# Kernel tuning notes

Hardware: AMD Instinct MI355X
Metric: run time of the kernel (lower is better)

Reference implementation:

```python
import jax, jax.numpy as jnp
import numpy as np

B, N, K = 32, 64, 128          # batch, atoms per cell, channel width (128x0e + 128x1o)
R_MAX = 5.0
NUM_BESSEL = 8
P_CUT = 5                       # num_polynomial_cutoff
AVG_NEIGH = 16.0                # avg_num_neighbors
H_MLP = 512                     # hidden_dimensions_size, n_hidden_dimensions = 2
FEAT = 5 * K                    # ((num_interactions-1)*4 + 1) * 128 = 640


def silu(x):
    return x * jax.nn.sigmoid(x)


def _bessel_cutoff(r, mask):
    # Bessel radial basis * polynomial cutoff (MACE), masked on valid edges.
    n = jnp.arange(1, NUM_BESSEL + 1, dtype=r.dtype)
    rb = jnp.sqrt(2.0 / R_MAX) * jnp.sin(n * (jnp.pi / R_MAX) * r[..., None]) / r[..., None]
    u = r / R_MAX
    p = float(P_CUT)
    fc = 1.0 - 0.5 * (p + 1) * (p + 2) * u**P_CUT + p * (p + 2) * u**(P_CUT + 1) - 0.5 * p * (p + 1) * u**(P_CUT + 2)
    fc = fc * (u < 1.0)
    return rb * (fc * mask)[..., None]


def _sph(uvec):
    # Real spherical harmonics l=0,1,2 (component normalization), uvec: unit edge vectors.
    x, y, z = uvec[..., 0], uvec[..., 1], uvec[..., 2]
    s3, s5, s15 = 3.0**0.5, 5.0**0.5, 15.0**0.5
    Y0 = jnp.ones_like(x)[..., None]
    Y1 = jnp.stack([s3 * x, s3 * y, s3 * z], -1)
    Y2 = jnp.stack([s15 * x * y, s15 * y * z, 0.5 * s5 * (3 * z * z - 1.0),
                    s15 * x * z, 0.5 * s15 * (x * x - y * y)], -1)
    return Y0, Y1, Y2


def _radial_mlp(x, w0, b0, w1, b1, w2, b2, w3, b3):
    h = silu(x @ w0 + b0)
    h = silu(h @ w1 + b1)
    h = silu(h @ w2 + b2)
    return h @ w3 + b3


def setup_inputs() -> dict:
    key = jax.random.key(0)
    ks = jax.random.split(key, 32)
    f32 = jnp.float32

    def lin(k, fan_in, shape):
        return (jax.random.normal(k, shape, dtype=f32) / np.sqrt(fan_in)).astype(f32)

    inp = {
        "noisy_relative_positions": jax.random.uniform(ks[0], (B, N, 3), dtype=f32),
        "time": jax.random.uniform(ks[1], (B, 1), dtype=f32),
        "unit_cell": (11.0 * jnp.eye(3, dtype=f32) + 0.3 * jax.random.uniform(ks[2], (B, 3, 3), dtype=f32)),
        "w_embed": lin(ks[3], 1, (K,)),
        # interaction 1 radial MLP: 8 -> 64 -> 64 -> 64 -> 3*K (weights for l=0,1,2 paths)
        "r1_w0": lin(ks[4], NUM_BESSEL, (NUM_BESSEL, 64)), "r1_b0": jnp.zeros((64,), f32),
        "r1_w1": lin(ks[5], 64, (64, 64)), "r1_b1": jnp.zeros((64,), f32),
        "r1_w2": lin(ks[6], 64, (64, 64)), "r1_b2": jnp.zeros((64,), f32),
        "r1_w3": lin(ks[7], 64, (64, 3 * K)), "r1_b3": jnp.zeros((3 * K,), f32),
        "mix1_l0": lin(ks[8], K, (K, K)),
        "mix1_l1": lin(ks[9], K, (K, K)),
        "mix1_l2": lin(ks[10], K, (K, K)),
        # interaction 2 radial MLP: 8 -> 64 -> 64 -> 64 -> 2*K (paths 0e x 0e -> 0e, 1o x 1o -> 0e)
        "r2_w0": lin(ks[11], NUM_BESSEL, (NUM_BESSEL, 64)), "r2_b0": jnp.zeros((64,), f32),
        "r2_w1": lin(ks[12], 64, (64, 64)), "r2_b1": jnp.zeros((64,), f32),
        "r2_w2": lin(ks[13], 64, (64, 64)), "r2_b2": jnp.zeros((64,), f32),
        "r2_w3": lin(ks[14], 64, (64, 2 * K)), "r2_b3": jnp.zeros((2 * K,), f32),
        "mix2": lin(ks[15], K, (K, K)),
        # readout MLP: 641 -> 512 -> 512 -> 3
        "mlp_w0": lin(ks[16], FEAT + 1, (FEAT + 1, H_MLP)), "mlp_b0": jnp.zeros((H_MLP,), f32),
        "mlp_w1": lin(ks[17], H_MLP, (H_MLP, H_MLP)), "mlp_b1": jnp.zeros((H_MLP,), f32),
        "mlp_w2": lin(ks[18], H_MLP, (H_MLP, 3)), "mlp_b2": jnp.zeros((3,), f32),
    }
    return inp


def reference(noisy_relative_positions, time, unit_cell, w_embed,
              r1_w0, r1_b0, r1_w1, r1_b1, r1_w2, r1_b2, r1_w3, r1_b3,
              mix1_l0, mix1_l1, mix1_l2,
              r2_w0, r2_b0, r2_w1, r2_b1, r2_w2, r2_b2, r2_w3, r2_b3, mix2,
              mlp_w0, mlp_b0, mlp_w1, mlp_b1, mlp_w2, mlp_b2):
    frac = noisy_relative_positions                      # [B,N,3] fractional
    d = frac[:, :, None, :] - frac[:, None, :, :]        # [B,N,N,3]
    d = d - jnp.round(d)                                 # minimum-image PBC
    dc = jnp.einsum('bijc,bcd->bijd', d, unit_cell)      # cartesian displacements
    r = jnp.sqrt(jnp.maximum(jnp.sum(dc * dc, -1), 1e-12))
    mask = (r < R_MAX) & (~jnp.eye(N, dtype=bool))[None]
    r_safe = jnp.where(mask, r, 1.0)
    uvec = dc / r_safe[..., None] * mask[..., None]      # unit edge vectors (0 off-edge)

    rad = _bessel_cutoff(r_safe, mask)                   # [B,N,N,8]
    Y0, Y1, Y2 = _sph(uvec)                              # [B,N,N,1|3|5]

    h0 = jnp.broadcast_to(w_embed, (B, N, K))            # element embedding (single species)

    # ---- interaction 1: radial-weighted tensor product h_j (x) Y_l, scatter over j ----
    we = _radial_mlp(rad, r1_w0, r1_b0, r1_w1, r1_b1, r1_w2, r1_b2, r1_w3, r1_b3)
    we = we.reshape(B, N, N, 3, K) * mask[..., None, None]
    hj = h0[:, None, :, :]                               # sender features [B,1,N,K]
    msg0 = jnp.einsum('bijk,bijm->bimk', we[..., 0, :] * hj, Y0)[:, :, 0] / AVG_NEIGH  # [B,N,K]
    msg1 = jnp.einsum('bijk,bijm->bimk', we[..., 1, :] * hj, Y1) / AVG_NEIGH           # [B,N,3,K]
    msg2 = jnp.einsum('bijk,bijm->bimk', we[..., 2, :] * hj, Y2) / AVG_NEIGH           # [B,N,5,K]

    s1 = msg0 @ mix1_l0 + jnp.sum(msg2 * msg2, axis=2) @ mix1_l2   # scalars [B,N,K]
    v1 = jnp.einsum('bimk,kc->bimc', msg1, mix1_l1)                # vectors [B,N,3,K]
    h1 = silu(s1)

    # ---- interaction 2: scalar output from 0e x 0e and 1o x 1o -> 0e paths ----
    we2 = _radial_mlp(rad, r2_w0, r2_b0, r2_w1, r2_b1, r2_w2, r2_b2, r2_w3, r2_b3)
    we2 = we2.reshape(B, N, N, 2, K) * mask[..., None, None]
    msg_a = jnp.sum(we2[..., 0, :] * h1[:, None, :, :], axis=2)    # [B,N,K]
    inv = jnp.einsum('bijm,bjmk->bijk', Y1, v1)                    # Y1 . v1_j invariant
    msg_b = jnp.sum(we2[..., 1, :] * inv, axis=2)
    s2 = ((msg_a + msg_b) / AVG_NEIGH) @ mix2                      # [B,N,K]

    # node_feats: layer1 full irreps (128x0e + 128x1o -> 512) + layer2 scalars (128) = 640
    node_feats = jnp.concatenate([s1, v1.reshape(B, N, 3 * K), s2], axis=-1)

    t = jnp.broadcast_to(time[:, None, :], (B, N, 1))
    x = jnp.concatenate([node_feats, t], axis=-1)                  # [B,N,641]
    x = jax.nn.relu(x @ mlp_w0 + mlp_b0)
    x = jax.nn.relu(x @ mlp_w1 + mlp_b1)
    return x @ mlp_w2 + mlp_b2                                     # [B,N,3]
```

## Files before the change

kernel.cpp:

```cpp
#include <hip/hip_runtime.h>
#include <math.h>

#define B_ 32
#define N_ 64
#define K_ 128
#define NPAIR (B_*N_*N_)
#define PREP_TOTAL 733184

typedef __attribute__((ext_vector_type(8))) short short8;
typedef __attribute__((ext_vector_type(8))) __bf16 bf16x8;
typedef __attribute__((ext_vector_type(4))) float floatx4;

__device__ __forceinline__ float silu_f(float x) {
    return x / (1.0f + expf(-x));
}

__device__ __forceinline__ short f2bf(float x) {
    union { float f; unsigned u; } v; v.f = x;
    unsigned r = (v.u + 0x7FFFu + ((v.u >> 16) & 1u)) >> 16;
    return (short)r;
}
__device__ __forceinline__ float bf2f(short s) {
    union { unsigned u; float f; } v;
    v.u = ((unsigned)(unsigned short)s) << 16;
// ... 54 lines not shown
}

__global__ __launch_bounds__(256) void geom_kernel(
    const float* __restrict__ pos, const float* __restrict__ cell,
    float* __restrict__ rad, float* __restrict__ Y1, float* __restrict__ Y2,
    float* __restrict__ maskf)
{
    int p = blockIdx.x * 256 + threadIdx.x;
    if (p >= NPAIR) return;
    int b = p >> 12;
    int ij = p & 4095;
    int i = ij >> 6, j = ij & 63;
    const float* pi = pos + (size_t)(b*N_ + i)*3;
    const float* pj = pos + (size_t)(b*N_ + j)*3;
    float d0 = pi[0]-pj[0], d1 = pi[1]-pj[1], d2 = pi[2]-pj[2];
    d0 -= rintf(d0); d1 -= rintf(d1); d2 -= rintf(d2);
    const float* C = cell + b*9;
    float dc0 = d0*C[0] + d1*C[3] + d2*C[6];
    float dc1 = d0*C[1] + d1*C[4] + d2*C[7];
    float dc2 = d0*C[2] + d1*C[5] + d2*C[8];
    float r2 = fmaxf(dc0*dc0 + dc1*dc1 + dc2*dc2, 1e-12f);
    float r = sqrtf(r2);
    bool m = (r < 5.0f) && (i != j);
    float mf = m ? 1.0f : 0.0f;
    float rs = m ? r : 1.0f;
    float inv_rs = 1.0f / rs;
    float x = dc0*inv_rs*mf, y = dc1*inv_rs*mf, z = dc2*inv_rs*mf;
    float u = r * 0.2f;
    float u2 = u*u, u4 = u2*u2, u5 = u4*u;
    float fc = 1.0f - 21.0f*u5 + 35.0f*u5*u - 15.0f*u5*u2;
    fc = (u < 1.0f) ? fc : 0.0f;
    float pref = 0.6324555320336759f * inv_rs * (fc * mf);
    float w = 0.6283185307179586f * rs;
    #pragma unroll
    for (int n = 1; n <= 8; n++)
        rad[(size_t)p*8 + (n-1)] = pref * sinf((float)n * w);
    const float s3  = 1.7320508075688772f;
    const float s5  = 2.23606797749979f;
    const float s15 = 3.872983346207417f;
    float* y1 = Y1 + (size_t)p*3;
    y1[0] = s3*x; y1[1] = s3*y; y1[2] = s3*z;
    float* y2 = Y2 + (size_t)p*5;
    y2[0] = s15*x*y;
    y2[1] = s15*y*z;
    y2[2] = 0.5f*s5*(3.0f*z*z - 1.0f);
    y2[3] = s15*x*z;
    y2[4] = 0.5f*s15*(x*x - y*y);
    maskf[p] = mf;
}

__device__ __forceinline__ void mfma_layer(
    const short* __restrict__ src, const short* __restrict__ WT,
    const float* __restrict__ bias, short* __restrict__ dst,
    int wv, int qd, int nn)
{
    floatx4 acc[4];
    #pragma unroll
    for (int tt = 0; tt < 4; tt++) acc[tt] = (floatx4){0.f, 0.f, 0.f, 0.f};
    #pragma unroll
    for (int ks = 0; ks < 64; ks += 32) {
        bf16x8 a = ld_frag(&src[(wv*16 + nn)*72 + ks + qd*8]);
        #pragma unroll
        for (int tt = 0; tt < 4; tt++) {
            bf16x8 b = ld_frag(&WT[(tt*16 + nn)*64 + ks + qd*8]);
            acc[tt] = __builtin_amdgcn_mfma_f32_16x16x32_bf16(a, b, acc[tt], 0, 0, 0);
        }
    }
    #pragma unroll
    for (int tt = 0; tt < 4; tt++) {
        int col = tt*16 + nn;
        float bv = bias[col];
        #pragma unroll
        for (int i = 0; i < 4; i++) {
            int row = wv*16 + qd*4 + i;
            dst[row*72 + col] = f2bf(silu_f(acc[tt][i] + bv));
        }
    }
}

__device__ __forceinline__ void mfma_layer_T(
    const short* __restrict__ src, const short* __restrict__ WT,
    const float* __restrict__ bias, short* __restrict__ dstT,
    int wv, int qd, int nn)
{
    floatx4 acc[4];
    #pragma unroll
    for (int tt = 0; tt < 4; tt++) acc[tt] = (floatx4){0.f, 0.f, 0.f, 0.f};
    #pragma unroll
    for (int ks = 0; ks < 64; ks += 32) {
        bf16x8 a = ld_frag(&src[(wv*16 + nn)*72 + ks + qd*8]);
        #pragma unroll
        for (int tt = 0; tt < 4; tt++) {
            bf16x8 b = ld_frag(&WT[(tt*16 + nn)*64 + ks + qd*8]);
            acc[tt] = __builtin_amdgcn_mfma_f32_16x16x32_bf16(a, b, acc[tt], 0, 0, 0);
        }
    }
    #pragma unroll
    for (int tt = 0; tt < 4; tt++) {
        int col = tt*16 + nn;
        float bv = bias[col];
        #pragma unroll
        for (int i = 0; i < 4; i++) {
            int row = wv*16 + qd*4 + i;
            dstT[col*72 + row] = f2bf(silu_f(acc[tt][i] + bv));
        }
    }
}

__device__ __forceinline__ void mfma_layer0(
    const short* __restrict__ rad_bf, const short* __restrict__ w0T,
    const float* __restrict__ b0, short* __restrict__ dst,
    int wv, int qd, int nn)
{
    floatx4 acc[4];
    #pragma unroll
    for (int tt = 0; tt < 4; tt++) acc[tt] = (floatx4){0.f, 0.f, 0.f, 0.f};
    bf16x8 a = ld_frag(&rad_bf[(wv*16 + nn)*40 + qd*8]);
    #pragma unroll
    for (int tt = 0; tt < 4; tt++) {
        bf16x8 b = ld_frag(&w0T[(tt*16 + nn)*32 + qd*8]);
        acc[tt] = __builtin_amdgcn_mfma_f32_16x16x32_bf16(a, b, acc[tt], 0, 0, 0);
    }
    #pragma unroll
    for (int tt = 0; tt < 4; tt++) {
        int col = tt*16 + nn;
        float bv = b0[col];
        #pragma unroll
        for (int i = 0; i < 4; i++) {
            int row = wv*16 + qd*4 + i;
            dst[row*72 + col] = f2bf(silu_f(acc[tt][i] + bv));
        }
    }
}

__global__ __launch_bounds__(256) void pass1_kernel(
    const float* __restrict__ rad, const float* __restrict__ Y1g,
    const float* __restrict__ Y2g, const float* __restrict__ maskg,
    const float* __restrict__ wemb,
    const short* __restrict__ w0T, const float* __restrict__ b0,
    const short* __restrict__ w1T, const float* __restrict__ b1,
    const short* __restrict__ w2T, const float* __restrict__ b2,
    const short* __restrict__ w3T, const float* __restrict__ b3,
    const short* __restrict__ lcatT, const float* __restrict__ timeg,
    float* __restrict__ h1g, float* __restrict__ v1g, short* __restrict__ featsb)
{
    __shared__ __align__(16) short lds_a[2560];
    __shared__ __align__(16) short actA[64*72];
    __shared__ __align__(16) short actB[64*72];
    __shared__ __align__(16) short Ym_bf[16*72];
    __shared__ __align__(16) short G_bf[16*72];
    __shared__ __align__(16) float msg[1152];
    __shared__ float SY[9];
    __shared__ float q_s[128];
    int t = threadIdx.x;
    int wv = t >> 6, lane = t & 63, qd = lane >> 4, nn = lane & 15;
    int node = blockIdx.x;
    int b = node >> 6;
    size_t pbase = (size_t)node * 64;

    for (int idx = t; idx < 2048; idx += 256) {
        int j = idx >> 5, k = idx & 31;
        lds_a[j*40 + k] = (k < 8) ? f2bf(rad[pbase*8 + j*8 + k]) : (short)0;
    }
    if (t < 64) {
        int j = t;
        float mf = maskg[pbase + j];
        float vals[9];
        vals[0] = mf;
        #pragma unroll
        for (int m = 0; m < 3; m++) vals[1+m] = Y1g[(pbase+j)*3 + m] * mf;
        #pragma unroll
        for (int m = 0; m < 5; m++) vals[4+m] = Y2g[(pbase+j)*5 + m] * mf;
        #pragma unroll
        for (int m = 0; m < 9; m++) Ym_bf[m*72 + j] = f2bf(vals[m]);
        #pragma unroll
        for (int m = 9; m < 16; m++) Ym_bf[m*72 + j] = 0;
        #pragma unroll
        for (int m = 0; m < 9; m++) {
            float s = vals[m];
            #pragma unroll
            for (int off = 32; off > 0; off >>= 1) s += __shfl_xor(s, off);
            if (j == 0) SY[m] = s;
        }
    }
    __syncthreads();

    mfma_layer0(lds_a, w0T, b0, actA, wv, qd, nn);
    __syncthreads();
    mfma_layer(actA, w1T, b1, actB, wv, qd, nn);
    __syncthreads();
    mfma_layer_T(actB, w2T, b2, actA, wv, qd, nn);
    __syncthreads();

    {
        floatx4 acc = (floatx4){0.f, 0.f, 0.f, 0.f};
        #pragma unroll
        for (int ks = 0; ks < 64; ks += 32) {
            bf16x8 a = ld_frag(&Ym_bf[nn*72 + ks + qd*8]);
            bf16x8 bb = ld_frag(&actA[(wv*16 + nn)*72 + ks + qd*8]);
            acc = __builtin_amdgcn_mfma_f32_16x16x32_bf16(a, bb, acc, 0, 0, 0);
        }
        #pragma unroll
        for (int i = 0; i < 4; i++)
            G_bf[(qd*4 + i)*72 + wv*16 + nn] = f2bf(acc[i]);
    }
    __syncthreads();

    {
        floatx4 acc[6];
        #pragma unroll
        for (int tt = 0; tt < 6; tt++) acc[tt] = (floatx4){0.f, 0.f, 0.f, 0.f};
        #pragma unroll
        for (int ks = 0; ks < 64; ks += 32) {
            bf16x8 a = ld_frag(&G_bf[nn*72 + ks + qd*8]);
            #pragma unroll
            for (int tt = 0; tt < 6; tt++) {
                bf16x8 bb = ld_frag(&w3T[((wv*6 + tt)*16 + nn)*64 + ks + qd*8]);
                acc[tt] = __builtin_amdgcn_mfma_f32_16x16x32_bf16(a, bb, acc[tt], 0, 0, 0);
            }
        }
        #pragma unroll
        for (int tt = 0; tt < 6; tt++) {
            int col = (wv*6 + tt)*16 + nn;
            #pragma unroll
            for (int i = 0; i < 4; i++) {
                int m = qd*4 + i;
                if (m < 9) {
                    int c = (m == 0) ? 0 : ((m < 4) ? 1 : 2);
                    int k = col - c*128;
                    if (k >= 0 && k < 128)
                        msg[m*128 + k] = (acc[tt][i] + SY[m]*b3[col]) * wemb[k] * 0.0625f;
                }
            }
        }
    }
    __syncthreads();

    if (t < 128) {
        int k = t;
        float acc = 0.f;
        #pragma unroll
        for (int m = 4; m < 9; m++) { float v = msg[m*128 + k]; acc += v*v; }
        q_s[k] = acc;
    }
    __syncthreads();

    for (int idx = t; idx < 2048; idx += 256) {
        int r = idx >> 7, k = idx & 127;
        float v = (r == 0) ? msg[k]
                : (r == 1) ? q_s[k]
                : (r < 5)  ? msg[(r-1)*128 + k] : 0.f;
        lds_a[r*136 + k] = f2bf(v);
    }
    __syncthreads();

    {
        floatx4 acc[6];
        #pragma unroll
        for (int tt = 0; tt < 6; tt++) acc[tt] = (floatx4){0.f, 0.f, 0.f, 0.f};
        #pragma unroll
        for (int ks = 0; ks < 128; ks += 32) {
            bf16x8 a = ld_frag(&lds_a[nn*136 + ks + qd*8]);
            #pragma unroll
            for (int tt = 0; tt < 6; tt++) {
                bf16x8 bb = ld_frag(&lcatT[((size_t)((wv*6 + tt)*16 + nn))*128 + ks + qd*8]);
                acc[tt] = __builtin_amdgcn_mfma_f32_16x16x32_bf16(a, bb, acc[tt], 0, 0, 0);
            }
        }
        float* Ps_a = msg;
        float* Ps_b = msg + 128;
        float* Pv   = msg + 256;
        #pragma unroll
        for (int tt = 0; tt < 6; tt++) {
            int n = (wv*6 + tt)*16 + nn;
            #pragma unroll
            for (int i = 0; i < 4; i++) {
                int r = qd*4 + i;
                float val = acc[tt][i];
                if (r == 0 && n < 128) Ps_a[n] = val;
                else if (r == 1 && n >= 256) Ps_b[n - 256] = val;
                else if (r >= 2 && r < 5 && n >= 128 && n < 256)
                    Pv[(r-2)*128 + (n-128)] = val;
            }
        }
    }
    __syncthreads();

    for (int idx = t; idx < 512; idx += 256) {
        if (idx < 128) {
            int c = idx;
            float s1 = msg[c] + msg[128 + c];
            featsb[(size_t)node*704 + c] = f2bf(s1);
            h1g[(size_t)node*128 + c] = silu_f(s1);
        } else {
            int vi = idx - 128;
            int m = vi >> 7, c = vi & 127;
            float v = msg[256 + m*128 + c];
            v1g[(size_t)node*384 + m*128 + c] = v;
            featsb[(size_t)node*704 + 128 + m*128 + c] = f2bf(v);
        }
    }
    if (t == 0) featsb[(size_t)node*704 + 640] = f2bf(timeg[b]);
    if (t < 63) featsb[(size_t)node*704 + 641 + t] = 0;
}

__global__ __launch_bounds__(256) void pass2_kernel(
    const float* __restrict__ rad, const float* __restrict__ Y1g,
    const float* __restrict__ maskg,
    const short* __restrict__ w0T, const float* __restrict__ b0,
    const short* __restrict__ w1T, const float* __restrict__ b1,
    const short* __restrict__ w2T, const float* __restrict__ b2,
    const short* __restrict__ w3T, const float* __restrict__ b3,
    const float* __restrict__ mix2,
    const float* __restrict__ h1g, const float* __restrict__ v1g,
    short* __restrict__ featsb)
{
    __shared__ __align__(16) short rad_bf[2560];
    __shared__ __align__(16) short actA[64*72];
    __shared__ __align__(16) short actB[64*72];
    __shared__ float Y1s[64*4];
    __shared__ float mask_s[64];
    __shared__ float msgab[128];
    int t = threadIdx.x;
    int wv = t >> 6, lane = t & 63, qd = lane >> 4, nn = lane & 15;
    int node = blockIdx.x;
    int b = node >> 6;
    size_t pbase = (size_t)node * 64;

    for (int idx = t; idx < 2048; idx += 256) {
        int j = idx >> 5, k = idx & 31;
        rad_bf[j*40 + k] = (k < 8) ? f2bf(rad[pbase*8 + j*8 + k]) : (short)0;
    }
    if (t < 64) {
        mask_s[t] = maskg[pbase + t];
        #pragma unroll
        for (int m = 0; m < 3; m++) Y1s[t*4 + m] = Y1g[(pbase+t)*3 + m];
    }
    if (t < 128) msgab[t] = 0.f;
    __syncthreads();

    mfma_layer0(rad_bf, w0T, b0, actA, wv, qd, nn);
    __syncthreads();
    mfma_layer(actA, w1T, b1, actB, wv, qd, nn);
    __syncthreads();
    mfma_layer(actB, w2T, b2, actA, wv, qd, nn);
    __syncthreads();

    for (int g = 0; g < 4; g++) {
        floatx4 acc[4];
        #pragma unroll
        for (int tt = 0; tt < 4; tt++) acc[tt] = (floatx4){0.f, 0.f, 0.f, 0.f};
        #pragma unroll
        for (int ks = 0; ks < 64; ks += 32) {
            bf16x8 a = ld_frag(&actA[(wv*16 + nn)*72 + ks + qd*8]);
            #pragma unroll
            for (int tt = 0; tt < 4; tt++) {
                int col0 = g*64 + tt*16;
                bf16x8 bb = ld_frag(&w3T[(col0 + nn)*64 + ks + qd*8]);
                acc[tt] = __builtin_amdgcn_mfma_f32_16x16x32_bf16(a, bb, acc[tt], 0, 0, 0);
            }
        }
        #pragma unroll
        for (int tt = 0; tt < 4; tt++) {
            int col = g*64 + tt*16 + nn;
            float bias = b3[col];
            int k = col & 127;
            float p = 0.f;
            if (col < 128) {
                #pragma unroll
                for (int i = 0; i < 4; i++) {
                    int j = wv*16 + qd*4 + i;
                    float we = (acc[tt][i] + bias) * mask_s[j];
                    p += we * h1g[((size_t)b*64 + j)*128 + k];
                }
            } else {
                #pragma unroll
                for (int i = 0; i < 4; i++) {
                    int j = wv*16 + qd*4 + i;
                    float we = (acc[tt][i] + bias) * mask_s[j];
                    const float* vb = &v1g[((size_t)b*64 + j)*384 + k];
                    float inv = Y1s[j*4+0]*vb[0] + Y1s[j*4+1]*vb[128] + Y1s[j*4+2]*vb[256];
                    p += we * inv;
                }
            }
            p += __shfl_xor(p, 16);
            p += __shfl_xor(p, 32);
            if (qd == 0) atomicAdd(&msgab[k], p);
        }
    }
    __syncthreads();

    if (t < 128) {
        int c = t;
        float acc = 0.f;
        for (int k = 0; k < 128; k++) acc += msgab[k] * mix2[k*128 + c];
        featsb[(size_t)node*704 + 512 + c] = f2bf(acc * 0.0625f);
    }
}

__global__ __launch_bounds__(256) void gemm_mfma_kernel(
    const short* __restrict__ A, int lda,
    const short* __restrict__ BT, int ldb, int K,
    const float* __restrict__ bias, short* __restrict__ Cout, int ldo)
{
    __shared__ short As[64*72];
    __shared__ short Bs[64*72];
    int t = threadIdx.x;
    int wv = t >> 6, lane = t & 63, qd = lane >> 4, nn = lane & 15;
    int m0 = blockIdx.x * 64, n0 = blockIdx.y * 64;
    floatx4 acc[4];
    #pragma unroll
    for (int tt = 0; tt < 4; tt++) acc[tt] = (floatx4){0.f, 0.f, 0.f, 0.f};

    for (int kc = 0; kc < K; kc += 64) {
        for (int s = t; s < 512; s += 256) {
            int j = s >> 3, kk = (s & 7) * 8;
            *(uint4*)&As[j*72 + kk] = *(const uint4*)&A[(size_t)(m0 + j)*lda + kc + kk];
            *(uint4*)&Bs[j*72 + kk] = *(const uint4*)&BT[(size_t)(n0 + j)*ldb + kc + kk];
        }
        __syncthreads();
        #pragma unroll
        for (int ks = 0; ks < 64; ks += 32) {
            bf16x8 a = ld_frag(&As[(wv*16 + nn)*72 + ks + qd*8]);
            #pragma unroll
            for (int tt = 0; tt < 4; tt++) {
                bf16x8 bb = ld_frag(&Bs[(tt*16 + nn)*72 + ks + qd*8]);
// ... 65 lines not shown
    const float* r2b1  = (const float*)d_in[18];
    const float* r2w2  = (const float*)d_in[19];
    const float* r2b2  = (const float*)d_in[20];
    const float* r2w3  = (const float*)d_in[21];
    const float* r2b3  = (const float*)d_in[22];
    const float* mix2  = (const float*)d_in[23];
    const float* mw0   = (const float*)d_in[24];
    const float* mb0   = (const float*)d_in[25];
    const float* mw1   = (const float*)d_in[26];
    const float* mb1   = (const float*)d_in[27];
    const float* mw2   = (const float*)d_in[28];
    const float* mb2   = (const float*)d_in[29];

    float* ws    = (float*)d_ws;
    float* rad   = ws;
    float* Y1    = rad   + (size_t)NPAIR*8;
    float* Y2    = Y1    + (size_t)NPAIR*3;
    float* maskf = Y2    + (size_t)NPAIR*5;
    float* h1    = maskf + (size_t)NPAIR;
    float* v1    = h1    + (size_t)B_*N_*K_;
    short* featsb = (short*)(v1 + (size_t)B_*N_*3*K_);
    short* prep  = featsb + (size_t)2048*704;
    short* w1T_1 = prep;
    short* w2T_1 = prep + 4096;
    short* w1T_2 = prep + 8192;
    short* w2T_2 = prep + 12288;
    short* w3T_2 = prep + 16384;
    short* wT0   = prep + 32768;
    short* wT1   = prep + 393216;
    short* w0T_1 = prep + 655360;
    short* w0T_2 = prep + 657408;
    short* w3T_1 = prep + 659456;
    short* lcatT = prep + 684032;
    short* h0bb = (short*)rad;
    short* h1bb = (short*)Y2;

    prep_kernel<<<(PREP_TOTAL + 255)/256, 256, 0, stream>>>(
        r1w1, r1w2, r2w1, r2w2, r2w3, mw0, mw1,
        r1w0, r2w0, r1w3, l0, l1, l2, prep);
    geom_kernel<<<NPAIR/256, 256, 0, stream>>>(pos, cell, rad, Y1, Y2, maskf);
    pass1_kernel<<<B_*N_, 256, 0, stream>>>(rad, Y1, Y2, maskf, wemb,
        w0T_1, r1b0, w1T_1, r1b1, w2T_1, r1b2, w3T_1, r1b3, lcatT, timeg,
        h1, v1, featsb);
    pass2_kernel<<<B_*N_, 256, 0, stream>>>(rad, Y1, maskf,
        w0T_2, r2b0, w1T_2, r2b1, w2T_2, r2b2, w3T_2, r2b3, mix2, h1, v1, featsb);
    dim3 g0(32, 8);
    gemm_mfma_kernel<<<g0, 256, 0, stream>>>(featsb, 704, wT0, 704, 704, mb0, h0bb, 512);
    gemm_mfma_kernel<<<g0, 256, 0, stream>>>(h0bb, 512, wT1, 512, 512, mb1, h1bb, 512);
    final3_kernel<<<B_*N_, 64, 0, stream>>>(h1bb, mw2, mb2, (float*)d_out);
}
```

Measured before the change: 289.2 us.

## Split pass kernels into MLP and per-wave back-end kernels via global buffer

Each of the two interaction pass kernels is split into an MLP kernel, which computes the first three radial MLP layers per node and writes the hidden activations to a global bf16 buffer, and a back-end kernel that handles four nodes per block with one wave per node and no block-level barriers. In back2 the shared-memory atomics are replaced by per-lane register accumulation. The aim is to remove __syncthreads stalls and idle waves in the serial tail stages. The cost is an extra round trip of the hidden activations through global memory, two more kernel launches, and repeated weight-fragment loads per wave.

```diff
diff --git a/kernel.cpp b/kernel.cpp
--- a/kernel.cpp
+++ b/kernel.cpp
@@ -156,35 +156,6 @@
     }
 }
 
-__device__ __forceinline__ void mfma_layer_T(
-    const short* __restrict__ src, const short* __restrict__ WT,
-    const float* __restrict__ bias, short* __restrict__ dstT,
-    int wv, int qd, int nn)
-{
-    floatx4 acc[4];
-    #pragma unroll
-    for (int tt = 0; tt < 4; tt++) acc[tt] = (floatx4){0.f, 0.f, 0.f, 0.f};
-    #pragma unroll
-    for (int ks = 0; ks < 64; ks += 32) {
-        bf16x8 a = ld_frag(&src[(wv*16 + nn)*72 + ks + qd*8]);
-        #pragma unroll
-        for (int tt = 0; tt < 4; tt++) {
-            bf16x8 b = ld_frag(&WT[(tt*16 + nn)*64 + ks + qd*8]);
-            acc[tt] = __builtin_amdgcn_mfma_f32_16x16x32_bf16(a, b, acc[tt], 0, 0, 0);
-        }
-    }
-    #pragma unroll
-    for (int tt = 0; tt < 4; tt++) {
-        int col = tt*16 + nn;
-        float bv = bias[col];
-        #pragma unroll
-        for (int i = 0; i < 4; i++) {
-            int row = wv*16 + qd*4 + i;
-            dstT[col*72 + row] = f2bf(silu_f(acc[tt][i] + bv));
-        }
-    }
-}
-
 __device__ __forceinline__ void mfma_layer0(
     const short* __restrict__ rad_bf, const short* __restrict__ w0T,
     const float* __restrict__ b0, short* __restrict__ dst,
@@ -211,37 +182,91 @@
     }
 }
 
-__global__ __launch_bounds__(256) void pass1_kernel(
-    const float* __restrict__ rad, const float* __restrict__ Y1g,
-    const float* __restrict__ Y2g, const float* __restrict__ maskg,
-    const float* __restrict__ wemb,
+template<int TR>
+__global__ __launch_bounds__(256) void mlp_kernel(
+    const float* __restrict__ rad,
     const short* __restrict__ w0T, const float* __restrict__ b0,
     const short* __restrict__ w1T, const float* __restrict__ b1,
     const short* __restrict__ w2T, const float* __restrict__ b2,
+    short* __restrict__ hcOut)
+{
+    __shared__ __align__(16) short rad_bf[2560];
+    __shared__ __align__(16) short actA[64*72];
+    __shared__ __align__(16) short actB[64*72];
+    int t = threadIdx.x;
+    int wv = t >> 6, lane = t & 63, qd = lane >> 4, nn = lane & 15;
+    int node = blockIdx.x;
+    size_t pbase = (size_t)node * 64;
+
+    for (int idx = t; idx < 2048; idx += 256) {
+        int j = idx >> 5, k = idx & 31;
+        rad_bf[j*40 + k] = (k < 8) ? f2bf(rad[pbase*8 + j*8 + k]) : (short)0;
+    }
+    __syncthreads();
+    mfma_layer0(rad_bf, w0T, b0, actA, wv, qd, nn);
+    __syncthreads();
+    mfma_layer(actA, w1T, b1, actB, wv, qd, nn);
+    __syncthreads();
+
+    floatx4 acc[4];
+    #pragma unroll
+    for (int tt = 0; tt < 4; tt++) acc[tt] = (floatx4){0.f, 0.f, 0.f, 0.f};
+    #pragma unroll
+    for (int ks = 0; ks < 64; ks += 32) {
+        bf16x8 a = ld_frag(&actB[(wv*16 + nn)*72 + ks + qd*8]);
+        #pragma unroll
+        for (int tt = 0; tt < 4; tt++) {
+            bf16x8 b = ld_frag(&w2T[(tt*16 + nn)*64 + ks + qd*8]);
+            acc[tt] = __builtin_amdgcn_mfma_f32_16x16x32_bf16(a, b, acc[tt], 0, 0, 0);
+        }
+    }
+    #pragma unroll
+    for (int tt = 0; tt < 4; tt++) {
+        int col = tt*16 + nn;
+        float bv = b2[col];
+        if (TR) {
+            short4 v;
+            v.x = f2bf(silu_f(acc[tt][0] + bv));
+            v.y = f2bf(silu_f(acc[tt][1] + bv));
+            v.z = f2bf(silu_f(acc[tt][2] + bv));
+            v.w = f2bf(silu_f(acc[tt][3] + bv));
+            *(short4*)&hcOut[(size_t)node*4096 + col*64 + wv*16 + qd*4] = v;
+        } else {
+            #pragma unroll
+            for (int i = 0; i < 4; i++) {
+                int row = wv*16 + qd*4 + i;
+                hcOut[(size_t)node*4096 + row*64 + col] = f2bf(silu_f(acc[tt][i] + bv));
+            }
+        }
+    }
+}
+
+#define W1_SIZE 6816
+__global__ __launch_bounds__(256) void back1_kernel(
+    const float* __restrict__ Y1g, const float* __restrict__ Y2g,
+    const float* __restrict__ maskg, const float* __restrict__ wemb,
+    const short* __restrict__ hcT,
     const short* __restrict__ w3T, const float* __restrict__ b3,
     const short* __restrict__ lcatT, const float* __restrict__ timeg,
     float* __restrict__ h1g, float* __restrict__ v1g, short* __restrict__ featsb)
 {
-    __shared__ __align__(16) short lds_a[2560];
-    __shared__ __align__(16) short actA[64*72];
-    __shared__ __align__(16) short actB[64*72];
-    __shared__ __align__(16) short Ym_bf[16*72];
-    __shared__ __align__(16) short G_bf[16*72];
-    __shared__ __align__(16) float msg[1152];
-    __shared__ float SY[9];
-    __shared__ float q_s[128];
+    __shared__ __align__(16) short sdata[4*W1_SIZE];
     int t = threadIdx.x;
     int wv = t >> 6, lane = t & 63, qd = lane >> 4, nn = lane & 15;
-    int node = blockIdx.x;
+    int node = blockIdx.x*4 + wv;
     int b = node >> 6;
     size_t pbase = (size_t)node * 64;
-
-    for (int idx = t; idx < 2048; idx += 256) {
-        int j = idx >> 5, k = idx & 31;
-        lds_a[j*40 + k] = (k < 8) ? f2bf(rad[pbase*8 + j*8 + k]) : (short)0;
-    }
-    if (t < 64) {
-        int j = t;
+    short* sw  = sdata + wv*W1_SIZE;
+    short* Ym  = sw;
+    short* Gbf = sw + 1152;
+    short* A2  = sw + 2304;
+    float* msg = (float*)(sw + 4480);
+    float* SYl = (float*)(sw + 6784);
+    float* Psa = msg;
+    float* Psb = msg + 128;
+
+    {
+        int j = lane;
         float mf = maskg[pbase + j];
         float vals[9];
         vals[0] = mf;
@@ -250,226 +275,224 @@
         #pragma unroll
         for (int m = 0; m < 5; m++) vals[4+m] = Y2g[(pbase+j)*5 + m] * mf;
         #pragma unroll
-        for (int m = 0; m < 9; m++) Ym_bf[m*72 + j] = f2bf(vals[m]);
-        #pragma unroll
-        for (int m = 9; m < 16; m++) Ym_bf[m*72 + j] = 0;
+        for (int m = 0; m < 9; m++) Ym[m*72 + j] = f2bf(vals[m]);
+        #pragma unroll
+        for (int m = 9; m < 16; m++) Ym[m*72 + j] = 0;
         #pragma unroll
         for (int m = 0; m < 9; m++) {
             float s = vals[m];
             #pragma unroll
             for (int off = 32; off > 0; off >>= 1) s += __shfl_xor(s, off);
-            if (j == 0) SY[m] = s;
-        }
-    }
-    __syncthreads();
-
-    mfma_layer0(lds_a, w0T, b0, actA, wv, qd, nn);
-    __syncthreads();
-    mfma_layer(actA, w1T, b1, actB, wv, qd, nn);
-    __syncthreads();
-    mfma_layer_T(actB, w2T, b2, actA, wv, qd, nn);
-    __syncthreads();
+            if (lane == m) SYl[m] = s;
+        }
+    }
 
     {
-        floatx4 acc = (floatx4){0.f, 0.f, 0.f, 0.f};
-        #pragma unroll
-        for (int ks = 0; ks < 64; ks += 32) {
-            bf16x8 a = ld_frag(&Ym_bf[nn*72 + ks + qd*8]);
-            bf16x8 bb = ld_frag(&actA[(wv*16 + nn)*72 + ks + qd*8]);
-            acc = __builtin_amdgcn_mfma_f32_16x16x32_bf16(a, bb, acc, 0, 0, 0);
-        }
-        #pragma unroll
-        for (int i = 0; i < 4; i++)
-            G_bf[(qd*4 + i)*72 + wv*16 + nn] = f2bf(acc[i]);
-    }
-    __syncthreads();
+        bf16x8 ya0 = ld_frag(&Ym[nn*72 + qd*8]);
+        bf16x8 ya1 = ld_frag(&Ym[nn*72 + 32 + qd*8]);
+        const short* hb = hcT + (size_t)node*4096 + nn*64 + qd*8;
+        #pragma unroll
+        for (int tn = 0; tn < 4; tn++) {
+            floatx4 acc = (floatx4){0.f, 0.f, 0.f, 0.f};
+            bf16x8 b0f = ld_frag(hb + tn*1024);
+            bf16x8 b1f = ld_frag(hb + tn*1024 + 32);
+            acc = __builtin_amdgcn_mfma_f32_16x16x32_bf16(ya0, b0f, acc, 0, 0, 0);
+            acc = __builtin_amdgcn_mfma_f32_16x16x32_bf16(ya1, b1f, acc, 0, 0, 0);
+            #pragma unroll
+            for (int i = 0; i < 4; i++)
+                Gbf[(qd*4 + i)*72 + tn*16 + nn] = f2bf(acc[i]);
+        }
+    }
 
     {
-        floatx4 acc[6];
-        #pragma unroll
-        for (int tt = 0; tt < 6; tt++) acc[tt] = (floatx4){0.f, 0.f, 0.f, 0.f};
-        #pragma unroll
-        for (int ks = 0; ks < 64; ks += 32) {
-            bf16x8 a = ld_frag(&G_bf[nn*72 + ks + qd*8]);
+        bf16x8 ga0 = ld_frag(&Gbf[nn*72 + qd*8]);
+        bf16x8 ga1 = ld_frag(&Gbf[nn*72 + 32 + qd*8]);
+        const short* wb = w3T + nn*64 + qd*8;
+        #pragma unroll
+        for (int g = 0; g < 4; g++) {
+            floatx4 acc[6];
+            #pragma unroll
+            for (int tt = 0; tt < 6; tt++) acc[tt] = (floatx4){0.f, 0.f, 0.f, 0.f};
             #pragma unroll
             for (int tt = 0; tt < 6; tt++) {
-                bf16x8 bb = ld_frag(&w3T[((wv*6 + tt)*16 + nn)*64 + ks + qd*8]);
-                acc[tt] = __builtin_amdgcn_mfma_f32_16x16x32_bf16(a, bb, acc[tt], 0, 0, 0);
-            }
-        }
-        #pragma unroll
-        for (int tt = 0; tt < 6; tt++) {
-            int col = (wv*6 + tt)*16 + nn;
-            #pragma unroll
-            for (int i = 0; i < 4; i++) {
-                int m = qd*4 + i;
-                if (m < 9) {
-                    int c = (m == 0) ? 0 : ((m < 4) ? 1 : 2);
-                    int k = col - c*128;
-                    if (k >= 0 && k < 128)
-                        msg[m*128 + k] = (acc[tt][i] + SY[m]*b3[col]) * wemb[k] * 0.0625f;
+                int tn = g*6 + tt;
+                bf16x8 b0f = ld_frag(wb + tn*1024);
+                bf16x8 b1f = ld_frag(wb + tn*1024 + 32);
+                acc[tt] = __builtin_amdgcn_mfma_f32_16x16x32_bf16(ga0, b0f, acc[tt], 0, 0, 0);
+                acc[tt] = __builtin_amdgcn_mfma_f32_16x16x32_bf16(ga1, b1f, acc[tt], 0, 0, 0);
+            }
+            #pragma unroll
+            for (int tt = 0; tt < 6; tt++) {
+                int col = (g*6 + tt)*16 + nn;
+                #pragma unroll
+                for (int i = 0; i < 4; i++) {
+                    int m = qd*4 + i;
+                    if (m < 9) {
+                        int c = (m == 0) ? 0 : ((m < 4) ? 1 : 2);
+                        int k = col - c*128;
+                        if (k >= 0 && k < 128)
+                            msg[m*128 + k] = (acc[tt][i] + SYl[m]*b3[col]) * wemb[k] * 0.0625f;
+                    }
                 }
             }
         }
     }
-    __syncthreads();
-
-    if (t < 128) {
-        int k = t;
-        float acc = 0.f;
-        #pragma unroll
-        for (int m = 4; m < 9; m++) { float v = msg[m*128 + k]; acc += v*v; }
-        q_s[k] = acc;
-    }
-    __syncthreads();
-
-    for (int idx = t; idx < 2048; idx += 256) {
-        int r = idx >> 7, k = idx & 127;
-        float v = (r == 0) ? msg[k]
-                : (r == 1) ? q_s[k]
-                : (r < 5)  ? msg[(r-1)*128 + k] : 0.f;
-        lds_a[r*136 + k] = f2bf(v);
-    }
-    __syncthreads();
 
     {
-        floatx4 acc[6];
-        #pragma unroll
-        for (int tt = 0; tt < 6; tt++) acc[tt] = (floatx4){0.f, 0.f, 0.f, 0.f};
-        #pragma unroll
-        for (int ks = 0; ks < 128; ks += 32) {
-            bf16x8 a = ld_frag(&lds_a[nn*136 + ks + qd*8]);
+        int c = lane*2;
+        float ma[9], mb[9];
+        #pragma unroll
+        for (int m = 0; m < 9; m++) { ma[m] = msg[m*128 + c]; mb[m] = msg[m*128 + c + 1]; }
+        float qa = 0.f, qb = 0.f;
+        #pragma unroll
+        for (int m = 4; m < 9; m++) { qa += ma[m]*ma[m]; qb += mb[m]*mb[m]; }
+        #pragma unroll
+        for (int r = 0; r < 16; r++) {
+            float va = (r == 0) ? ma[0] : (r == 1) ? qa : (r < 5) ? ma[r-1] : 0.f;
+            float vb = (r == 0) ? mb[0] : (r == 1) ? qb : (r < 5) ? mb[r-1] : 0.f;
+            *(short2*)&A2[r*136 + c] = make_short2(f2bf(va), f2bf(vb));
+        }
+    }
+
+    {
+        bf16x8 pa[4];
+        #pragma unroll
+        for (int ksI = 0; ksI < 4; ksI++)
+            pa[ksI] = ld_frag(&A2[nn*136 + ksI*32 + qd*8]);
+        const short* lb = lcatT + nn*128 + qd*8;
+        #pragma unroll
+        for (int g = 0; g < 4; g++) {
+            floatx4 acc[6];
+            #pragma unroll
+            for (int tt = 0; tt < 6; tt++) acc[tt] = (floatx4){0.f, 0.f, 0.f, 0.f};
             #pragma unroll
             for (int tt = 0; tt < 6; tt++) {
-                bf16x8 bb = ld_frag(&lcatT[((size_t)((wv*6 + tt)*16 + nn))*128 + ks + qd*8]);
-                acc[tt] = __builtin_amdgcn_mfma_f32_16x16x32_bf16(a, bb, acc[tt], 0, 0, 0);
-            }
-        }
-        float* Ps_a = msg;
-        float* Ps_b = msg + 128;
-        float* Pv   = msg + 256;
-        #pragma unroll
-        for (int tt = 0; tt < 6; tt++) {
-            int n = (wv*6 + tt)*16 + nn;
-            #pragma unroll
-            for (int i = 0; i < 4; i++) {
-                int r = qd*4 + i;
-                float val = acc[tt][i];
-                if (r == 0 && n < 128) Ps_a[n] = val;
-                else if (r == 1 && n >= 256) Ps_b[n - 256] = val;
-                else if (r >= 2 && r < 5 && n >= 128 && n < 256)
-                    Pv[(r-2)*128 + (n-128)] = val;
-            }
-        }
-    }
-    __syncthreads();
-
-    for (int idx = t; idx < 512; idx += 256) {
-        if (idx < 128) {
-            int c = idx;
-            float s1 = msg[c] + msg[128 + c];
-            featsb[(size_t)node*704 + c] = f2bf(s1);
-            h1g[(size_t)node*128 + c] = silu_f(s1);
-        } else {
-            int vi = idx - 128;
-            int m = vi >> 7, c = vi & 127;
-            float v = msg[256 + m*128 + c];
-            v1g[(size_t)node*384 + m*128 + c] = v;
-            featsb[(size_t)node*704 + 128 + m*128 + c] = f2bf(v);
-        }
-    }
-    if (t == 0) featsb[(size_t)node*704 + 640] = f2bf(timeg[b]);
-    if (t < 63) featsb[(size_t)node*704 + 641 + t] = 0;
-}
-
-__global__ __launch_bounds__(256) void pass2_kernel(
-    const float* __restrict__ rad, const float* __restrict__ Y1g,
-    const float* __restrict__ maskg,
-    const short* __restrict__ w0T, const float* __restrict__ b0,
-    const short* __restrict__ w1T, const float* __restrict__ b1,
-    const short* __restrict__ w2T, const float* __restrict__ b2,
+                int tn = g*6 + tt;
+                #pragma unroll
+                for (int ksI = 0; ksI < 4; ksI++) {
+                    bf16x8 bf = ld_frag(lb + tn*2048 + ksI*32);
+                    acc[tt] = __builtin_amdgcn_mfma_f32_16x16x32_bf16(pa[ksI], bf, acc[tt], 0, 0, 0);
+                }
+            }
+            #pragma unroll
+            for (int tt = 0; tt < 6; tt++) {
+                int n = (g*6 + tt)*16 + nn;
+                #pragma unroll
+                for (int i = 0; i < 4; i++) {
+                    int r = qd*4 + i;
+                    float val = acc[tt][i];
+                    if (r == 0 && n < 128) Psa[n] = val;
+                    else if (r == 1 && n >= 256) Psb[n - 256] = val;
+                    else if (r >= 2 && r < 5 && n >= 128 && n < 256) {
+                        int m = r - 2, cc = n - 128;
+                        v1g[(size_t)node*384 + m*128 + cc] = val;
+                        featsb[(size_t)node*704 + 128 + m*128 + cc] = f2bf(val);
+                    }
+                }
+            }
+        }
+    }
+
+    {
+        int c = lane*2;
+        #pragma unroll
+        for (int d = 0; d < 2; d++) {
+            float s1 = Psa[c+d] + Psb[c+d];
+            featsb[(size_t)node*704 + c + d] = f2bf(s1);
+            h1g[(size_t)node*128 + c + d] = silu_f(s1);
+        }
+        if (lane == 0) featsb[(size_t)node*704 + 640] = f2bf(timeg[b]);
+        if (lane < 63) featsb[(size_t)node*704 + 641 + lane] = 0;
+    }
+}
+
+__global__ __launch_bounds__(256) void back2_kernel(
+    const float* __restrict__ Y1g, const float* __restrict__ maskg,
+    const short* __restrict__ hc2,
     const short* __restrict__ w3T, const float* __restrict__ b3,
     const float* __restrict__ mix2,
     const float* __restrict__ h1g, const float* __restrict__ v1g,
     short* __restrict__ featsb)
 {
-    __shared__ __align__(16) short rad_bf[2560];
-    __shared__ __align__(16) short actA[64*72];
-    __shared__ __align__(16) short actB[64*72];
-    __shared__ float Y1s[64*4];
-    __shared__ float mask_s[64];
-    __shared__ float msgab[128];
+    __shared__ float sdataf[4*448];
     int t = threadIdx.x;
     int wv = t >> 6, lane = t & 63, qd = lane >> 4, nn = lane & 15;
-    int node = blockIdx.x;
+    int node = blockIdx.x*4 + wv;
     int b = node >> 6;
     size_t pbase = (size_t)node * 64;
-
-    for (int idx = t; idx < 2048; idx += 256) {
-        int j = idx >> 5, k = idx & 31;
-        rad_bf[j*40 + k] = (k < 8) ? f2bf(rad[pbase*8 + j*8 + k]) : (short)0;
-    }
-    if (t < 64) {
-        mask_s[t] = maskg[pbase + t];
-        #pragma unroll
-        for (int m = 0; m < 3; m++) Y1s[t*4 + m] = Y1g[(pbase+t)*3 + m];
-    }
-    if (t < 128) msgab[t] = 0.f;
-    __syncthreads();
-
-    mfma_layer0(rad_bf, w0T, b0, actA, wv, qd, nn);
-    __syncthreads();
-    mfma_layer(actA, w1T, b1, actB, wv, qd, nn);
-    __syncthreads();
-    mfma_layer(actB, w2T, b2, actA, wv, qd, nn);
-    __syncthreads();
-
-    for (int g = 0; g < 4; g++) {
-        floatx4 acc[4];
-        #pragma unroll
-        for (int tt = 0; tt < 4; tt++) acc[tt] = (floatx4){0.f, 0.f, 0.f, 0.f};
-        #pragma unroll
-        for (int ks = 0; ks < 64; ks += 32) {
-            bf16x8 a = ld_frag(&actA[(wv*16 + nn)*72 + ks + qd*8]);
+    float* fw     = sdataf + wv*448;
+    float* mask_s = fw;
+    float* Y1s    = fw + 64;
+    float* msgab  = fw + 320;
+
+    {
+        int j = lane;
+        mask_s[j] = maskg[pbase + j];
+        #pragma unroll
+        for (int m = 0; m < 3; m++) Y1s[j*4 + m] = Y1g[(pbase+j)*3 + m];
+    }
+
+    float mreg[8];
+    #pragma unroll
+    for (int cc = 0; cc < 8; cc++) mreg[cc] = 0.f;
+
+    const short* ab = hc2 + (size_t)node*4096 + nn*64 + qd*8;
+    const short* wb = w3T + nn*64 + qd*8;
+    #pragma unroll
+    for (int mt = 0; mt < 4; mt++) {
+        bf16x8 a0 = ld_frag(ab + mt*1024);
+        bf16x8 a1 = ld_frag(ab + mt*1024 + 32);
+        #pragma unroll
+        for (int cg = 0; cg < 4; cg++) {
+            floatx4 acc[4];
+            #pragma unroll
+            for (int tt = 0; tt < 4; tt++) acc[tt] = (floatx4){0.f, 0.f, 0.f, 0.f};
             #pragma unroll
             for (int tt = 0; tt < 4; tt++) {
-                int col0 = g*64 + tt*16;
-                bf16x8 bb = ld_frag(&w3T[(col0 + nn)*64 + ks + qd*8]);
-                acc[tt] = __builtin_amdgcn_mfma_f32_16x16x32_bf16(a, bb, acc[tt], 0, 0, 0);
-            }
-        }
-        #pragma unroll
-        for (int tt = 0; tt < 4; tt++) {
-            int col = g*64 + tt*16 + nn;
-            float bias = b3[col];
-            int k = col & 127;
-            float p = 0.f;
-            if (col < 128) {
-                #pragma unroll
-                for (int i = 0; i < 4; i++) {
-                    int j = wv*16 + qd*4 + i;
-                    float we = (acc[tt][i] + bias) * mask_s[j];
-                    p += we * h1g[((size_t)b*64 + j)*128 + k];
+                int ct = cg*4 + tt;
+                bf16x8 b0f = ld_frag(wb + ct*1024);
+                bf16x8 b1f = ld_frag(wb + ct*1024 + 32);
+                acc[tt] = __builtin_amdgcn_mfma_f32_16x16x32_bf16(a0, b0f, acc[tt], 0, 0, 0);
+                acc[tt] = __builtin_amdgcn_mfma_f32_16x16x32_bf16(a1, b1f, acc[tt], 0, 0, 0);
+            }
+            #pragma unroll
+            for (int tt = 0; tt < 4; tt++) {
+                int ct = cg*4 + tt;
+                int col = ct*16 + nn;
+                float bias = b3[col];
+                int k = col & 127;
+                float p = 0.f;
+                if (col < 128) {
+                    #pragma unroll
+                    for (int i = 0; i < 4; i++) {
+                        int j = mt*16 + qd*4 + i;
+                        float we = (acc[tt][i] + bias) * mask_s[j];
+                        p += we * h1g[((size_t)b*64 + j)*128 + k];
+                    }
+                } else {
+                    #pragma unroll
+                    for (int i = 0; i < 4; i++) {
+                        int j = mt*16 + qd*4 + i;
+                        float we = (acc[tt][i] + bias) * mask_s[j];
+                        const float* vb2 = &v1g[((size_t)b*64 + j)*384 + k];
+                        float inv = Y1s[j*4+0]*vb2[0] + Y1s[j*4+1]*vb2[128] + Y1s[j*4+2]*vb2[256];
+                        p += we * inv;
+                    }
                 }
-            } else {
-                #pragma unroll
-                for (int i = 0; i < 4; i++) {
-                    int j = wv*16 + qd*4 + i;
-                    float we = (acc[tt][i] + bias) * mask_s[j];
-                    const float* vb = &v1g[((size_t)b*64 + j)*384 + k];
-                    float inv = Y1s[j*4+0]*vb[0] + Y1s[j*4+1]*vb[128] + Y1s[j*4+2]*vb[256];
-                    p += we * inv;
-                }
-            }
-            p += __shfl_xor(p, 16);
-            p += __shfl_xor(p, 32);
-            if (qd == 0) atomicAdd(&msgab[k], p);
-        }
-    }
-    __syncthreads();
-
-    if (t < 128) {
-        int c = t;
+                p += __shfl_xor(p, 16);
+                p += __shfl_xor(p, 32);
+                mreg[ct & 7] += p;
+            }
+        }
+    }
+
+    if (qd == 0) {
+        #pragma unroll
+        for (int cc = 0; cc < 8; cc++) msgab[cc*16 + nn] = mreg[cc];
+    }
+    #pragma unroll
+    for (int half = 0; half < 2; half++) {
+        int c = half*64 + lane;
         float acc = 0.f;
         for (int k = 0; k < 128; k++) acc += msgab[k] * mix2[k*128 + c];
         featsb[(size_t)node*704 + 512 + c] = f2bf(acc * 0.0625f);
@@ -601,6 +624,7 @@
     short* w0T_2 = prep + 657408;
     short* w3T_1 = prep + 659456;
     short* lcatT = prep + 684032;
+    short* hcbuf = prep + PREP_TOTAL;
     short* h0bb = (short*)rad;
     short* h1bb = (short*)Y2;
 
@@ -608,11 +632,12 @@
         r1w1, r1w2, r2w1, r2w2, r2w3, mw0, mw1,
         r1w0, r2w0, r1w3, l0, l1, l2, prep);
     geom_kernel<<<NPAIR/256, 256, 0, stream>>>(pos, cell, rad, Y1, Y2, maskf);
-    pass1_kernel<<<B_*N_, 256, 0, stream>>>(rad, Y1, Y2, maskf, wemb,
-        w0T_1, r1b0, w1T_1, r1b1, w2T_1, r1b2, w3T_1, r1b3, lcatT, timeg,
-        h1, v1, featsb);
-    pass2_kernel<<<B_*N_, 256, 0, stream>>>(rad, Y1, maskf,
-        w0T_2, r2b0, w1T_2, r2b1, w2T_2, r2b2, w3T_2, r2b3, mix2, h1, v1, featsb);
+    mlp_kernel<1><<<B_*N_, 256, 0, stream>>>(rad, w0T_1, r1b0, w1T_1, r1b1, w2T_1, r1b2, hcbuf);
+    back1_kernel<<<B_*N_/4, 256, 0, stream>>>(Y1, Y2, maskf, wemb, hcbuf,
+        w3T_1, r1b3, lcatT, timeg, h1, v1, featsb);
+    mlp_kernel<0><<<B_*N_, 256, 0, stream>>>(rad, w0T_2, r2b0, w1T_2, r2b1, w2T_2, r2b2, hcbuf);
+    back2_kernel<<<B_*N_/4, 256, 0, stream>>>(Y1, maskf, hcbuf,
+        w3T_2, r2b3, mix2, h1, v1, featsb);
     dim3 g0(32, 8);
     gemm_mfma_kernel<<<g0, 256, 0, stream>>>(featsb, 704, wT0, 704, 704, mb0, h0bb, 512);
     gemm_mfma_kernel<<<g0, 256, 0, stream>>>(h0bb, 512, wT1, 512, 512, mb1, h1bb, 512);
```

Measured after the change: 401.0 us. 38.6% more time.

## Alias shared-memory buffers, use sine recurrence, and write vector outputs directly

Applied to the files above, without the earlier changes.

Both per-node kernels now carve their LDS arrays out of one aliased byte buffer, reusing regions whose lifetimes do not overlap. This shrinks shared memory per block so more blocks can be resident per CU. The Bessel basis replaces eight sinf calls with one sin/cos pair and a Chebyshev recurrence. Pass1 also hoists the A-fragments of the lcat GEMM into registers and writes v1 and featsb straight from the accumulators instead of staging them through LDS. The aliasing relies on careful barrier placement, e.g. Ym_bf overlapping rad_bf, and the recurrence can accumulate slightly more rounding error.

```diff
diff --git a/kernel.cpp b/kernel.cpp
--- a/kernel.cpp
+++ b/kernel.cpp
@@ -110,9 +110,15 @@
     fc = (u < 1.0f) ? fc : 0.0f;
     float pref = 0.6324555320336759f * inv_rs * (fc * mf);
     float w = 0.6283185307179586f * rs;
-    #pragma unroll
-    for (int n = 1; n <= 8; n++)
-        rad[(size_t)p*8 + (n-1)] = pref * sinf((float)n * w);
+    float sw = sinf(w), cw = cosf(w);
+    float twoc = 2.0f * cw;
+    float sm = 0.0f, s = sw;
+    #pragma unroll
+    for (int n = 1; n <= 8; n++) {
+        rad[(size_t)p*8 + (n-1)] = pref * s;
+        float nx = twoc*s - sm;
+        sm = s; s = nx;
+    }
     const float s3  = 1.7320508075688772f;
     const float s5  = 2.23606797749979f;
     const float s15 = 3.872983346207417f;
@@ -193,7 +199,7 @@
     floatx4 acc[4];
     #pragma unroll
     for (int tt = 0; tt < 4; tt++) acc[tt] = (floatx4){0.f, 0.f, 0.f, 0.f};
-    bf16x8 a = ld_frag(&rad_bf[(wv*16 + nn)*40 + qd*8]);
+    bf16x8 a = ld_frag(&rad_bf[(wv*16 + nn)*32 + qd*8]);
     #pragma unroll
     for (int tt = 0; tt < 4; tt++) {
         bf16x8 b = ld_frag(&w0T[(tt*16 + nn)*32 + qd*8]);
@@ -222,14 +228,18 @@
     const short* __restrict__ lcatT, const float* __restrict__ timeg,
     float* __restrict__ h1g, float* __restrict__ v1g, short* __restrict__ featsb)
 {
-    __shared__ __align__(16) short lds_a[2560];
-    __shared__ __align__(16) short actA[64*72];
-    __shared__ __align__(16) short actB[64*72];
-    __shared__ __align__(16) short Ym_bf[16*72];
-    __shared__ __align__(16) short G_bf[16*72];
-    __shared__ __align__(16) float msg[1152];
-    __shared__ float SY[9];
-    __shared__ float q_s[128];
+    __shared__ __align__(16) char smem[23040];
+    short* actA   = (short*)smem;
+    short* actB   = (short*)(smem + 9216);
+    float* msg    = (float*)(smem + 9216);
+    float* q_s    = (float*)(smem + 9216 + 4608);
+    short* rad_bf = (short*)(smem + 18432);
+    short* Ym_bf  = (short*)(smem + 18432);
+    short* G_bf   = (short*)(smem + 18432 + 2304);
+    short* A2     = (short*)smem;
+    float* Psa    = (float*)(smem + 9216);
+    float* Psb    = Psa + 128;
+
     int t = threadIdx.x;
     int wv = t >> 6, lane = t & 63, qd = lane >> 4, nn = lane & 15;
     int node = blockIdx.x;
@@ -238,35 +248,44 @@
 
     for (int idx = t; idx < 2048; idx += 256) {
         int j = idx >> 5, k = idx & 31;
-        lds_a[j*40 + k] = (k < 8) ? f2bf(rad[pbase*8 + j*8 + k]) : (short)0;
-    }
+        rad_bf[j*32 + k] = (k < 8) ? f2bf(rad[pbase*8 + j*8 + k]) : (short)0;
+    }
+    float vals[9];
+    float sy9[9];
     if (t < 64) {
         int j = t;
         float mf = maskg[pbase + j];
-        float vals[9];
         vals[0] = mf;
         #pragma unroll
         for (int m = 0; m < 3; m++) vals[1+m] = Y1g[(pbase+j)*3 + m] * mf;
         #pragma unroll
         for (int m = 0; m < 5; m++) vals[4+m] = Y2g[(pbase+j)*5 + m] * mf;
-        #pragma unroll
-        for (int m = 0; m < 9; m++) Ym_bf[m*72 + j] = f2bf(vals[m]);
-        #pragma unroll
-        for (int m = 9; m < 16; m++) Ym_bf[m*72 + j] = 0;
         #pragma unroll
         for (int m = 0; m < 9; m++) {
             float s = vals[m];
             #pragma unroll
             for (int off = 32; off > 0; off >>= 1) s += __shfl_xor(s, off);
-            if (j == 0) SY[m] = s;
-        }
-    }
-    __syncthreads();
-
-    mfma_layer0(lds_a, w0T, b0, actA, wv, qd, nn);
-    __syncthreads();
+            sy9[m] = s;
+        }
+    }
+    __syncthreads();
+
+    mfma_layer0(rad_bf, w0T, b0, actA, wv, qd, nn);
+    __syncthreads();
+
+    if (t < 64) {
+        int j = t;
+        #pragma unroll
+        for (int m = 0; m < 9; m++) Ym_bf[m*72 + j] = f2bf(vals[m]);
+        #pragma unroll
+        for (int m = 9; m < 16; m++) Ym_bf[m*72 + j] = 0;
+        #pragma unroll
+        for (int m = 0; m < 9; m++)
+            if (j == m) *(float*)(&Ym_bf[m*72 + 64]) = sy9[m];
+    }
     mfma_layer(actA, w1T, b1, actB, wv, qd, nn);
     __syncthreads();
+
     mfma_layer_T(actB, w2T, b2, actA, wv, qd, nn);
     __syncthreads();
 
@@ -306,8 +325,10 @@
                 if (m < 9) {
                     int c = (m == 0) ? 0 : ((m < 4) ? 1 : 2);
                     int k = col - c*128;
-                    if (k >= 0 && k < 128)
-                        msg[m*128 + k] = (acc[tt][i] + SY[m]*b3[col]) * wemb[k] * 0.0625f;
+                    if (k >= 0 && k < 128) {
+                        float sym = *(const float*)(&Ym_bf[m*72 + 64]);
+                        msg[m*128 + k] = (acc[tt][i] + sym*b3[col]) * wemb[k] * 0.0625f;
+                    }
                 }
             }
         }
@@ -328,26 +349,27 @@
         float v = (r == 0) ? msg[k]
                 : (r == 1) ? q_s[k]
                 : (r < 5)  ? msg[(r-1)*128 + k] : 0.f;
-        lds_a[r*136 + k] = f2bf(v);
+        A2[r*136 + k] = f2bf(v);
     }
     __syncthreads();
 
     {
+        bf16x8 pa[4];
+        #pragma unroll
+        for (int ksI = 0; ksI < 4; ksI++)
+            pa[ksI] = ld_frag(&A2[nn*136 + ksI*32 + qd*8]);
         floatx4 acc[6];
         #pragma unroll
         for (int tt = 0; tt < 6; tt++) acc[tt] = (floatx4){0.f, 0.f, 0.f, 0.f};
         #pragma unroll
-        for (int ks = 0; ks < 128; ks += 32) {
-            bf16x8 a = ld_frag(&lds_a[nn*136 + ks + qd*8]);
+        for (int tt = 0; tt < 6; tt++) {
+            int tn = wv*6 + tt;
             #pragma unroll
-            for (int tt = 0; tt < 6; tt++) {
-                bf16x8 bb = ld_frag(&lcatT[((size_t)((wv*6 + tt)*16 + nn))*128 + ks + qd*8]);
-                acc[tt] = __builtin_amdgcn_mfma_f32_16x16x32_bf16(a, bb, acc[tt], 0, 0, 0);
+            for (int ksI = 0; ksI < 4; ksI++) {
+                bf16x8 bf = ld_frag(&lcatT[((size_t)(tn*16 + nn))*128 + ksI*32 + qd*8]);
+                acc[tt] = __builtin_amdgcn_mfma_f32_16x16x32_bf16(pa[ksI], bf, acc[tt], 0, 0, 0);
             }
         }
-        float* Ps_a = msg;
-        float* Ps_b = msg + 128;
-        float* Pv   = msg + 256;
         #pragma unroll
         for (int tt = 0; tt < 6; tt++) {
             int n = (wv*6 + tt)*16 + nn;
@@ -355,31 +377,27 @@
             for (int i = 0; i < 4; i++) {
                 int r = qd*4 + i;
                 float val = acc[tt][i];
-                if (r == 0 && n < 128) Ps_a[n] = val;
-                else if (r == 1 && n >= 256) Ps_b[n - 256] = val;
-                else if (r >= 2 && r < 5 && n >= 128 && n < 256)
-                    Pv[(r-2)*128 + (n-128)] = val;
+                if (r == 0 && n < 128) Psa[n] = val;
+                else if (r == 1 && n >= 256) Psb[n - 256] = val;
+                else if (r >= 2 && r < 5 && n >= 128 && n < 256) {
+                    int m = r - 2, cc = n - 128;
+                    v1g[(size_t)node*384 + m*128 + cc] = val;
+                    featsb[(size_t)node*704 + 128 + m*128 + cc] = f2bf(val);
+                }
             }
         }
     }
     __syncthreads();
 
-    for (int idx = t; idx < 512; idx += 256) {
-        if (idx < 128) {
-            int c = idx;
-            float s1 = msg[c] + msg[128 + c];
-            featsb[(size_t)node*704 + c] = f2bf(s1);
-            h1g[(size_t)node*128 + c] = silu_f(s1);
-        } else {
-            int vi = idx - 128;
-            int m = vi >> 7, c = vi & 127;
-            float v = msg[256 + m*128 + c];
-            v1g[(size_t)node*384 + m*128 + c] = v;
-            featsb[(size_t)node*704 + 128 + m*128 + c] = f2bf(v);
-        }
-    }
-    if (t == 0) featsb[(size_t)node*704 + 640] = f2bf(timeg[b]);
-    if (t < 63) featsb[(size_t)node*704 + 641 + t] = 0;
+    if (t < 128) {
+        float s1 = Psa[t] + Psb[t];
+        featsb[(size_t)node*704 + t] = f2bf(s1);
+        h1g[(size_t)node*128 + t] = silu_f(s1);
+    } else if (t == 128) {
+        featsb[(size_t)node*704 + 640] = f2bf(timeg[b]);
+    } else if (t > 128 && t < 192) {
+        featsb[(size_t)node*704 + 640 + (t - 128)] = 0;
+    }
 }
 
 __global__ __launch_bounds__(256) void pass2_kernel(
@@ -393,12 +411,15 @@
     const float* __restrict__ h1g, const float* __restrict__ v1g,
     short* __restrict__ featsb)
 {
-    __shared__ __align__(16) short rad_bf[2560];
-    __shared__ __align__(16) short actA[64*72];
-    __shared__ __align__(16) short actB[64*72];
-    __shared__ float Y1s[64*4];
-    __shared__ float mask_s[64];
-    __shared__ float msgab[128];
+    __shared__ __align__(16) char smem[22528];
+    short* actA   = (short*)smem;
+    short* actB   = (short*)(smem + 9216);
+    short* rad_bf = (short*)(smem + 18432);
+    float* aux    = (float*)(smem + 18432);
+    float* mask_s = aux;
+    float* Y1s    = aux + 64;
+    float* msgab  = aux + 320;
+
     int t = threadIdx.x;
     int wv = t >> 6, lane = t & 63, qd = lane >> 4, nn = lane & 15;
     int node = blockIdx.x;
@@ -407,20 +428,28 @@
 
     for (int idx = t; idx < 2048; idx += 256) {
         int j = idx >> 5, k = idx & 31;
-        rad_bf[j*40 + k] = (k < 8) ? f2bf(rad[pbase*8 + j*8 + k]) : (short)0;
-    }
+        rad_bf[j*32 + k] = (k < 8) ? f2bf(rad[pbase*8 + j*8 + k]) : (short)0;
+    }
+    float pmf = 0.f, py0 = 0.f, py1 = 0.f, py2 = 0.f;
     if (t < 64) {
-        mask_s[t] = maskg[pbase + t];
-        #pragma unroll
-        for (int m = 0; m < 3; m++) Y1s[t*4 + m] = Y1g[(pbase+t)*3 + m];
+        pmf = maskg[pbase + t];
+        py0 = Y1g[(pbase+t)*3 + 0];
+        py1 = Y1g[(pbase+t)*3 + 1];
+        py2 = Y1g[(pbase+t)*3 + 2];
+    }
+    __syncthreads();
+
+    mfma_layer0(rad_bf, w0T, b0, actA, wv, qd, nn);
+    __syncthreads();
+
+    if (t < 64) {
+        mask_s[t] = pmf;
+        Y1s[t*4 + 0] = py0; Y1s[t*4 + 1] = py1; Y1s[t*4 + 2] = py2;
     }
     if (t < 128) msgab[t] = 0.f;
-    __syncthreads();
-
-    mfma_layer0(rad_bf, w0T, b0, actA, wv, qd, nn);
-    __syncthreads();
     mfma_layer(actA, w1T, b1, actB, wv, qd, nn);
     __syncthreads();
+
     mfma_layer(actB, w2T, b2, actA, wv, qd, nn);
     __syncthreads();
 
```

Result: no change. 290.2 us (+0.3%).
